# Performance work log

Measured on AMD Instinct MI355X. Metric: run time of the kernel, lower is better.

## Reference

```python
import jax, jax.numpy as jnp
import numpy as np

D_MODEL = 1024
N_HEADS = 16
D_K = D_MODEL // N_HEADS


def setup_inputs() -> dict:
    key = jax.random.key(0)
    ks = jax.random.split(key, 9)
    s = 1.0 / np.sqrt(D_MODEL)
    def lin(kw, kb):
        W = jax.random.uniform(kw, (D_MODEL, D_MODEL), jnp.float32, -s, s)
        b = jax.random.uniform(kb, (D_MODEL,), jnp.float32, -s, s)
        return W, b
    wq, bq = lin(ks[0], ks[1])
    wk, bk = lin(ks[2], ks[3])
    wv, bv = lin(ks[4], ks[5])
    wo, bo = lin(ks[6], ks[7])
    x = jax.random.normal(ks[8], (2, 2048, D_MODEL), jnp.float32)
    return {"x": x, "wq": wq, "bq": bq, "wk": wk, "bk": bk,
            "wv": wv, "bv": bv, "wo": wo, "bo": bo}


def reference(x, wq, bq, wk, bk, wv, bv, wo, bo):
    B, S, D = x.shape
    scale = 1.0 / np.sqrt(D_K)
    # projections (torch Linear: y = x W^T + b); W stored as [in,out] here
    q = x @ wq + bq
    k = x @ wk + bk
    v = x @ wv + bv
    # [B, H, S, d_k]
    q = q.reshape(B, S, N_HEADS, D_K).transpose(0, 2, 1, 3)
    k = k.reshape(B, S, N_HEADS, D_K).transpose(0, 2, 1, 3)
    v = v.reshape(B, S, N_HEADS, D_K).transpose(0, 2, 1, 3)
    scores = jnp.einsum('bhqd,bhkd->bhqk', q, k) * scale
    attn = jax.nn.softmax(scores, axis=-1)
    out = jnp.einsum('bhqk,bhkd->bhqd', attn, v)
    out = out.transpose(0, 2, 1, 3).reshape(B, S, D)
    return out @ wo + bo
```

## Files before the change

kernel.cpp:

```cpp
#include <hip/hip_runtime.h>
#include <hip/hip_bf16.h>
#include <math.h>

typedef __bf16 bf16x8 __attribute__((ext_vector_type(8)));
typedef unsigned short u16x8 __attribute__((ext_vector_type(8)));
typedef unsigned short u16x4 __attribute__((ext_vector_type(4)));
typedef float f32x4 __attribute__((ext_vector_type(4)));
typedef unsigned int u32x4 __attribute__((ext_vector_type(4)));
typedef unsigned int u32x2 __attribute__((ext_vector_type(2)));
typedef unsigned short u16;

__device__ __forceinline__ u16 f2bf(float f) {
    unsigned int x = __float_as_uint(f);
    x += 0x7fffu + ((x >> 16) & 1u);
    return (u16)(x >> 16);
}
__device__ __forceinline__ void glds16(const void* g, void* l) {
    __builtin_amdgcn_global_load_lds(
        (const __attribute__((address_space(1))) void*)g,
        (__attribute__((address_space(3))) void*)l, 16, 0, 0);
}
__device__ __forceinline__ void swap_half(unsigned& a, unsigned& b) {
    u32x2 t = __builtin_amdgcn_permlane32_swap(a, b, false, false);
    t = __builtin_amdgcn_permlane16_swap(t[0], t[1], false, false);
    a = t[0]; b = t[1];
}

__global__ __launch_bounds__(256) void prep(const float* __restrict__ W0, const float* __restrict__ W1,
                                            const float* __restrict__ W2, const float* __restrict__ W3,
                                            const float* __restrict__ X,
                                            u16* __restrict__ Wt, u16* __restrict__ Xb) {
    int z = blockIdx.z;
    if (z >= 4) {
        int row = (z - 4) * 1024 + blockIdx.y * 32 + blockIdx.x;
        const float* src = X + (size_t)row * 1024 + threadIdx.x * 4;
        f32x4 v = *(const f32x4*)src;
        u16x4 o; o[0] = f2bf(v[0]); o[1] = f2bf(v[1]); o[2] = f2bf(v[2]); o[3] = f2bf(v[3]);
        *(u16x4*)&Xb[(size_t)row * 1024 + threadIdx.x * 4] = o;
        return;
    }
    __shared__ float T[32][33];
    const float* W = (z == 0) ? W0 : ((z == 1) ? W1 : ((z == 2) ? W2 : W3));
    u16* dst = Wt + (size_t)z * 1024 * 1024;
    int k0 = blockIdx.y * 32, n0 = blockIdx.x * 32;
    int x = threadIdx.x & 31, y0 = threadIdx.x >> 5;
#pragma unroll
    for (int i = 0; i < 4; i++) {
        int y = y0 + i * 8;
        T[y][x] = W[(size_t)(k0 + y) * 1024 + n0 + x];
    }
    __syncthreads();
#pragma unroll
    for (int i = 0; i < 4; i++) {
        int y = y0 + i * 8;
        dst[(size_t)(n0 + y) * 1024 + k0 + x] = f2bf(T[x][y]);
    }
}

__global__ __launch_bounds__(512, 2) void gemm256(
    const u16* __restrict__ Bt,
    const float* __restrict__ b0, const float* __restrict__ b1, const float* __restrict__ b2,
    const u16* __restrict__ A, u16* __restrict__ C, u16* __restrict__ Vt)
{
    __shared__ __align__(16) u16 As[2][256 * 64];
    __shared__ __align__(16) u16 Bs[2][256 * 64];
    int tid = threadIdx.x;
    int lane = tid & 63, l15 = lane & 15, quad = lane >> 4;
    int wid = tid >> 6;
    int wm = wid >> 2, wn = wid & 3;
    int m0 = blockIdx.y * 256, n0 = blockIdx.x * 256;
    int sel = n0 >> 10;
    const float* bias = (sel == 0) ? b0 : ((sel == 1) ? b1 : b2);

    f32x4 acc[8][4];
#pragma unroll
    for (int i = 0; i < 8; i++)
#pragma unroll
        for (int j = 0; j < 4; j++) { f32x4 z = {0.f, 0.f, 0.f, 0.f}; acc[i][j] = z; }

    int rr = lane >> 3;
    int cc = (lane & 7) ^ rr;
    int fs7 = l15 & 7;
    const u16* abase = A  + (size_t)m0 * 1024;
    const u16* bbase = Bt + (size_t)n0 * 1024;

    auto stage = [&](int kt, int hp, int buf) {
        const u16* gsrc = (hp < 2) ? abase : bbase;
        u16* ldst = (hp < 2) ? As[buf] : Bs[buf];
        int k0 = kt * 64;
        int hbase = (hp & 1) * 128;
#pragma unroll
        for (int inst = 0; inst < 2; inst++) {
            int r0 = hbase + wid * 16 + inst * 8;
            glds16(&gsrc[(size_t)(r0 + rr) * 1024 + k0 + cc * 8], &ldst[r0 * 64]);
        }
    };

#pragma unroll
    for (int hp = 0; hp < 4; hp++) stage(0, hp, 0);

#pragma unroll 2
    for (int it = 0; it < 16; ++it) {
        int c = it & 1;
        if (it < 15) {
            stage(it + 1, 0, c ^ 1);
            asm volatile("s_waitcnt vmcnt(2)");
        } else {
            asm volatile("s_waitcnt vmcnt(0)");
        }
        __builtin_amdgcn_s_barrier();
        bf16x8 bfr[4][2];
#pragma unroll
        for (int nt = 0; nt < 4; nt++)
#pragma unroll
            for (int h = 0; h < 2; h++)
                bfr[nt][h] = *(const bf16x8*)&Bs[c][(wn * 64 + nt * 16 + l15) * 64 +
                                                    ((((h << 2) | quad) ^ fs7) * 8)];
        {
            bf16x8 af[2][2];
#pragma unroll
            for (int m = 0; m < 2; m++)
#pragma unroll
                for (int h = 0; h < 2; h++)
                    af[m][h] = *(const bf16x8*)&As[c][(wm * 128 + m * 16 + l15) * 64 +
                                                      ((((h << 2) | quad) ^ fs7) * 8)];
            asm volatile("s_waitcnt lgkmcnt(0)");
            __builtin_amdgcn_sched_barrier(0);
            __builtin_amdgcn_s_setprio(1);
#pragma unroll
            for (int m = 0; m < 2; m++)
#pragma unroll
                for (int nt = 0; nt < 4; nt++)
#pragma unroll
                    for (int h = 0; h < 2; h++)
                        acc[m][nt] = __builtin_amdgcn_mfma_f32_16x16x32_bf16(
                            af[m][h], bfr[nt][h], acc[m][nt], 0, 0, 0);
            __builtin_amdgcn_s_setprio(0);
            __builtin_amdgcn_s_barrier();
        }
#pragma unroll
        for (int p = 1; p < 4; p++) {
            bf16x8 af[2][2];
#pragma unroll
            for (int m = 0; m < 2; m++)
#pragma unroll
                for (int h = 0; h < 2; h++)
                    af[m][h] = *(const bf16x8*)&As[c][(wm * 128 + (p * 2 + m) * 16 + l15) * 64 +
                                                      ((((h << 2) | quad) ^ fs7) * 8)];
            if (it < 15) stage(it + 1, p, c ^ 1);
            __builtin_amdgcn_s_barrier();
            asm volatile("s_waitcnt lgkmcnt(0)");
            __builtin_amdgcn_sched_barrier(0);
            __builtin_amdgcn_s_setprio(1);
#pragma unroll
            for (int m = 0; m < 2; m++)
#pragma unroll
                for (int nt = 0; nt < 4; nt++)
#pragma unroll
                    for (int h = 0; h < 2; h++)
                        acc[p * 2 + m][nt] = __builtin_amdgcn_mfma_f32_16x16x32_bf16(
                            af[m][h], bfr[nt][h], acc[p * 2 + m][nt], 0, 0, 0);
            __builtin_amdgcn_s_setprio(0);
            __builtin_amdgcn_s_barrier();
        }
    }

    if (sel == 2) {
        int b = m0 >> 11;
#pragma unroll
        for (int mt = 0; mt < 8; mt++) {
            int gr = m0 + wm * 128 + mt * 16 + quad * 4;
            int s = gr & 2047;
#pragma unroll
            for (int nt = 0; nt < 4; nt++) {
                int gcl = (n0 & 1023) + wn * 64 + nt * 16 + l15;
                float bb = bias[gcl];
                u16x4 pk;
#pragma unroll
                for (int r = 0; r < 4; r++) pk[r] = f2bf(acc[mt][nt][r] + bb);
                *(u16x4*)&Vt[(size_t)((b * 16 + (gcl >> 6)) * 64 + (gcl & 63)) * 2048 + s] = pk;
            }
        }
        return;
    }
    float qs = (sel == 0) ? 0.18033688011112f : 1.0f;
#pragma unroll
    for (int mt = 0; mt < 8; mt++) {
        int gr = m0 + wm * 128 + mt * 16 + quad * 4;
#pragma unroll
        for (int nt = 0; nt < 4; nt++) {
            int gc = n0 + wn * 64 + nt * 16 + l15;
            float bb = bias[gc & 1023];
#pragma unroll
            for (int r = 0; r < 4; r++)
                C[(size_t)(gr + r) * 3072 + gc] = f2bf((acc[mt][nt][r] + bb) * qs);
        }
    }
}

template <bool OF32, bool VSPLIT>
__global__ __launch_bounds__(256) void gemm(
    const u16* __restrict__ Bt,
    const float* __restrict__ b0, const float* __restrict__ b1, const float* __restrict__ b2,
    const u16* __restrict__ A, void* __restrict__ Cptr, u16* __restrict__ Vt, int Ntot)
{
    __shared__ __align__(16) u16 As[128 * 32];
    __shared__ __align__(16) u16 Bs[128 * 32];
    int tid = threadIdx.x;
    int lane = tid & 63, l15 = lane & 15, quad = lane >> 4;
    int wid = tid >> 6, wm = wid >> 1, wn = wid & 1;
    int m0 = blockIdx.y * 128, n0 = blockIdx.x * 128;
    int sel = n0 >> 10;
    const float* bias = (sel == 0) ? b0 : ((sel == 1) ? b1 : b2);

    f32x4 acc[4][4];
#pragma unroll
    for (int i = 0; i < 4; i++)
#pragma unroll
        for (int j = 0; j < 4; j++) { f32x4 z = {0.f, 0.f, 0.f, 0.f}; acc[i][j] = z; }

    int rr = lane >> 2;
    int cc = (lane & 3) ^ ((rr >> 1) & 3);
    const u16* abase = A  + (size_t)m0 * 1024;
    const u16* bbase = Bt + (size_t)n0 * 1024;
    int fsw = (l15 >> 1) & 3;

    for (int k0 = 0; k0 < 1024; k0 += 32) {
#pragma unroll
        for (int inst = 0; inst < 2; inst++) {
            int r0 = wid * 32 + inst * 16;
            glds16(&abase[(size_t)(r0 + rr) * 1024 + k0 + cc * 8], &As[r0 * 32]);
            glds16(&bbase[(size_t)(r0 + rr) * 1024 + k0 + cc * 8], &Bs[r0 * 32]);
        }
        __syncthreads();
        bf16x8 af[4], bf[4];
#pragma unroll
        for (int mt = 0; mt < 4; mt++)
            af[mt] = *(const bf16x8*)&As[(wm * 64 + mt * 16 + l15) * 32 + ((quad ^ fsw) * 8)];
#pragma unroll
        for (int nt = 0; nt < 4; nt++)
            bf[nt] = *(const bf16x8*)&Bs[(wn * 64 + nt * 16 + l15) * 32 + ((quad ^ fsw) * 8)];
#pragma unroll
        for (int mt = 0; mt < 4; mt++)
#pragma unroll
            for (int nt = 0; nt < 4; nt++)
                acc[mt][nt] = __builtin_amdgcn_mfma_f32_16x16x32_bf16(af[mt], bf[nt], acc[mt][nt], 0, 0, 0);
        __syncthreads();
    }
    if (VSPLIT && sel == 2) {
        int b = m0 >> 11;
#pragma unroll
        for (int mt = 0; mt < 4; mt++) {
            int gr = m0 + wm * 64 + mt * 16 + quad * 4;
            int s = gr & 2047;
#pragma unroll
            for (int nt = 0; nt < 4; nt++) {
                int gcl = (n0 & 1023) + wn * 64 + nt * 16 + l15;
                float bb = bias[gcl];
                u16x4 pk;
#pragma unroll
                for (int r = 0; r < 4; r++) pk[r] = f2bf(acc[mt][nt][r] + bb);
                *(u16x4*)&Vt[(size_t)((b * 16 + (gcl >> 6)) * 64 + (gcl & 63)) * 2048 + s] = pk;
            }
        }
        return;
    }
    float qs = (VSPLIT && sel == 0) ? 0.18033688011112f : 1.0f;
#pragma unroll
    for (int mt = 0; mt < 4; mt++) {
        int gr = m0 + wm * 64 + mt * 16 + quad * 4;
#pragma unroll
        for (int nt = 0; nt < 4; nt++) {
            int gc = n0 + wn * 64 + nt * 16 + l15;
            float bb = bias[gc & 1023];
#pragma unroll
            for (int r = 0; r < 4; r++) {
                float v = (acc[mt][nt][r] + bb) * qs;
                if (OF32) ((float*)Cptr)[(size_t)(gr + r) * Ntot + gc] = v;
                else      ((u16*)Cptr)[(size_t)(gr + r) * Ntot + gc] = f2bf(v);
            }
        }
    }
}

__global__ __launch_bounds__(256, 2) void attn(const u16* __restrict__ QKV,
                                               const u16* __restrict__ Vt,
                                               u16* __restrict__ O)
{
    __shared__ __align__(16) u16 Ks[4][64 * 64];
    __shared__ __align__(16) u16 Vs[4][64 * 64];
    const int S = 2048, DQ = 3072;
    int tid = threadIdx.x, wid = tid >> 6, lane = tid & 63;
    int l15 = lane & 15, quad = lane >> 4;
    int lin = blockIdx.x;
    int xcd = lin & 7;
    int rest = lin >> 3;
    int qt = rest & 15;
    int g = xcd + 8 * (rest >> 4);
    int h = g & 15, b = g >> 4;
    const u16* base = QKV + (size_t)b * S * DQ + h * 64;
    const u16* Kb = base + 1024;
    const u16* Vtb = Vt + (size_t)((b * 16 + h) * 64) * 2048;
    int q0 = qt * 128 + wid * 32;

    bf16x8 qA0 = *(const bf16x8*)&base[(size_t)(q0 + l15) * DQ + quad * 8];
    bf16x8 qA1 = *(const bf16x8*)&base[(size_t)(q0 + l15) * DQ + 32 + quad * 8];
    bf16x8 qB0 = *(const bf16x8*)&base[(size_t)(q0 + 16 + l15) * DQ + quad * 8];
    bf16x8 qB1 = *(const bf16x8*)&base[(size_t)(q0 + 16 + l15) * DQ + 32 + quad * 8];

    f32x4 oA[4], oB[4];
#pragma unroll
    for (int i = 0; i < 4; i++) { f32x4 z = {0.f, 0.f, 0.f, 0.f}; oA[i] = z; oB[i] = z; }
    float psA = 0.f, psB = 0.f;

    int rr = lane >> 3;
    int cc = (lane & 7) ^ rr;
    int fs7 = l15 & 7;

    auto stage = [&](int it, int bsel) {
        int kv0 = it << 6;
#pragma unroll
        for (int inst = 0; inst < 2; inst++) {
            int r0 = wid * 16 + inst * 8;
            glds16(&Kb[(size_t)(kv0 + r0 + rr) * DQ + cc * 8], &Ks[bsel][r0 * 64]);
            glds16(&Vtb[(size_t)(r0 + rr) * 2048 + kv0 + cc * 8], &Vs[bsel][r0 * 64]);
        }
    };

    stage(0, 0);
    stage(1, 1);
    for (int it = 0; it < 32; ++it) {
        int cb = it & 3;
        if (it < 30) {
            stage(it + 2, (it + 2) & 3);
            asm volatile("s_waitcnt vmcnt(8)");
        } else if (it == 30) {
            asm volatile("s_waitcnt vmcnt(4)");
        } else {
            asm volatile("s_waitcnt vmcnt(0)");
        }
        __builtin_amdgcn_s_barrier();

        const u16* Kc = &Ks[cb][0];
        const u16* Vc = &Vs[cb][0];
        bf16x8 kfa[4], kfb[4], vfa[4], vfb[4];
#pragma unroll
        for (int t = 0; t < 4; t++) {
            kfa[t] = *(const bf16x8*)&Kc[(t * 16 + l15) * 64 + ((quad ^ fs7) * 8)];
            kfb[t] = *(const bf16x8*)&Kc[(t * 16 + l15) * 64 + (((quad + 4) ^ fs7) * 8)];
        }
#pragma unroll
        for (int dt = 0; dt < 4; dt++) {
            vfa[dt] = *(const bf16x8*)&Vc[(dt * 16 + l15) * 64 + ((quad ^ fs7) * 8)];
            vfb[dt] = *(const bf16x8*)&Vc[(dt * 16 + l15) * 64 + (((quad + 4) ^ fs7) * 8)];
        }

        f32x4 sA[4], sB[4];
#pragma unroll
        for (int t = 0; t < 4; t++) { f32x4 z = {0.f, 0.f, 0.f, 0.f}; sA[t] = z; sB[t] = z; }
        __builtin_amdgcn_s_setprio(1);
#pragma unroll
        for (int t = 0; t < 4; t++) {
            sA[t] = __builtin_amdgcn_mfma_f32_16x16x32_bf16(kfa[t], qA0, sA[t], 0, 0, 0);
            sA[t] = __builtin_amdgcn_mfma_f32_16x16x32_bf16(kfb[t], qA1, sA[t], 0, 0, 0);
            sB[t] = __builtin_amdgcn_mfma_f32_16x16x32_bf16(kfa[t], qB0, sB[t], 0, 0, 0);
            sB[t] = __builtin_amdgcn_mfma_f32_16x16x32_bf16(kfb[t], qB1, sB[t], 0, 0, 0);
        }
        __builtin_amdgcn_s_setprio(0);

        unsigned wA[4][2], wB[4][2];
#pragma unroll
        for (int t = 0; t < 4; t++) {
            float a0 = __builtin_amdgcn_exp2f(sA[t][0]);
            float a1 = __builtin_amdgcn_exp2f(sA[t][1]);
            float a2 = __builtin_amdgcn_exp2f(sA[t][2]);
            float a3 = __builtin_amdgcn_exp2f(sA[t][3]);
            psA += (a0 + a1) + (a2 + a3);
            asm("v_cvt_pk_bf16_f32 %0, %1, %2" : "=v"(wA[t][0]) : "v"(a0), "v"(a1));
            asm("v_cvt_pk_bf16_f32 %0, %1, %2" : "=v"(wA[t][1]) : "v"(a2), "v"(a3));
            float b0_ = __builtin_amdgcn_exp2f(sB[t][0]);
            float b1_ = __builtin_amdgcn_exp2f(sB[t][1]);
            float b2_ = __builtin_amdgcn_exp2f(sB[t][2]);
            float b3_ = __builtin_amdgcn_exp2f(sB[t][3]);
            psB += (b0_ + b1_) + (b2_ + b3_);
            asm("v_cvt_pk_bf16_f32 %0, %1, %2" : "=v"(wB[t][0]) : "v"(b0_), "v"(b1_));
            asm("v_cvt_pk_bf16_f32 %0, %1, %2" : "=v"(wB[t][1]) : "v"(b2_), "v"(b3_));
        }
        unsigned a0 = wA[0][0], a2 = wA[1][0]; swap_half(a0, a2);
        unsigned a1 = wA[0][1], a3 = wA[1][1]; swap_half(a1, a3);
        unsigned c0 = wA[2][0], c2 = wA[3][0]; swap_half(c0, c2);
        unsigned c1 = wA[2][1], c3 = wA[3][1]; swap_half(c1, c3);
        u32x4 pdA0 = {a0, a1, a2, a3};
        u32x4 pdA1 = {c0, c1, c2, c3};
        bf16x8 pfA0 = *(bf16x8*)&pdA0;
        bf16x8 pfA1 = *(bf16x8*)&pdA1;
        unsigned d0 = wB[0][0], d2 = wB[1][0]; swap_half(d0, d2);
        unsigned d1 = wB[0][1], d3 = wB[1][1]; swap_half(d1, d3);
        unsigned e0 = wB[2][0], e2 = wB[3][0]; swap_half(e0, e2);
        unsigned e1 = wB[2][1], e3 = wB[3][1]; swap_half(e1, e3);
        u32x4 pdB0 = {d0, d1, d2, d3};
        u32x4 pdB1 = {e0, e1, e2, e3};
        bf16x8 pfB0 = *(bf16x8*)&pdB0;
        bf16x8 pfB1 = *(bf16x8*)&pdB1;

        __builtin_amdgcn_s_setprio(1);
#pragma unroll
        for (int dt = 0; dt < 4; dt++) {
            oA[dt] = __builtin_amdgcn_mfma_f32_16x16x32_bf16(pfA0, vfa[dt], oA[dt], 0, 0, 0);
            oA[dt] = __builtin_amdgcn_mfma_f32_16x16x32_bf16(pfA1, vfb[dt], oA[dt], 0, 0, 0);
            oB[dt] = __builtin_amdgcn_mfma_f32_16x16x32_bf16(pfB0, vfa[dt], oB[dt], 0, 0, 0);
            oB[dt] = __builtin_amdgcn_mfma_f32_16x16x32_bf16(pfB1, vfb[dt], oB[dt], 0, 0, 0);
        }
        __builtin_amdgcn_s_setprio(0);
    }

    psA += __shfl_xor(psA, 16);
    psA += __shfl_xor(psA, 32);
    psB += __shfl_xor(psB, 16);
    psB += __shfl_xor(psB, 32);
#pragma unroll
    for (int r = 0; r < 4; r++) {
        float invA = 1.0f / __shfl(psA, quad * 4 + r);
        size_t rowA = (size_t)(b * S + q0 + quad * 4 + r);
#pragma unroll
        for (int dt = 0; dt < 4; dt++)
            O[rowA * 1024 + h * 64 + dt * 16 + l15] = f2bf(oA[dt][r] * invA);
        float invB = 1.0f / __shfl(psB, quad * 4 + r);
        size_t rowB = rowA + 16;
#pragma unroll
        for (int dt = 0; dt < 4; dt++)
            O[rowB * 1024 + h * 64 + dt * 16 + l15] = f2bf(oB[dt][r] * invB);
    }
}

extern "C" void kernel_launch(void* const* d_in, const int* in_sizes, int n_in,
                              void* d_out, int out_size, void* d_ws, size_t ws_size,
                              hipStream_t stream) {
    const float* x  = (const float*)d_in[0];
    const float* wq = (const float*)d_in[1];
    const float* bq = (const float*)d_in[2];
    const float* wk = (const float*)d_in[3];
    const float* bk = (const float*)d_in[4];
    const float* wv = (const float*)d_in[5];
    const float* bv = (const float*)d_in[6];
    const float* wo = (const float*)d_in[7];
    const float* bo = (const float*)d_in[8];
    float* out = (float*)d_out;

    u16* qkv  = (u16*)d_ws;
    u16* obuf = qkv  + (size_t)4096 * 3072;
    u16* vt   = obuf + (size_t)4096 * 1024;
    u16* wt   = vt   + (size_t)2048 * 2048;
    u16* xb   = wt   + (size_t)4 * 1024 * 1024;

    dim3 tb(256);
    prep<<<dim3(32, 32, 8), tb, 0, stream>>>(wq, wk, wv, wo, x, wt, xb);
    gemm256<<<dim3(12, 16), dim3(512), 0, stream>>>(wt, bq, bk, bv, xb, qkv, vt);
    attn<<<dim3(512), tb, 0, stream>>>(qkv, vt, obuf);
    gemm<true, false><<<dim3(8, 32), tb, 0, stream>>>(wt + (size_t)3 * 1024 * 1024,
                                                      bo, bo, bo, obuf, out, (u16*)nullptr, 1024);
}
```

Before: 193.2 us.

## Software-pipeline QK^T of next KV tile with softmax and PV of current tile

Splits the attention loop body into a QK^T stage and an exp/pack/PV stage, then interleaves them so the score MFMAs for tile i+1 are issued alongside the softmax and PV MFMAs for tile i. Two score accumulator sets alternate between even and odd tiles, and the loop is unrolled by two with a prologue and an epilogue. The aim is to hide the exp and permute latency and the MFMA dependency stalls behind independent matrix work. The cost is roughly double the score registers, which may lower occupancy, and more intricate waitcnt and barrier bookkeeping across the four LDS buffers.

```diff
diff --git a/kernel.cpp b/kernel.cpp
--- a/kernel.cpp
+++ b/kernel.cpp
@@ -317,8 +317,8 @@
     int cc = (lane & 7) ^ rr;
     int fs7 = l15 & 7;
 
-    auto stage = [&](int it, int bsel) {
-        int kv0 = it << 6;
+    auto stage = [&](int t) {
+        int kv0 = t << 6, bsel = t & 3;
 #pragma unroll
         for (int inst = 0; inst < 2; inst++) {
             int r0 = wid * 16 + inst * 8;
@@ -327,61 +327,49 @@
         }
     };
 
-    stage(0, 0);
-    stage(1, 1);
-    for (int it = 0; it < 32; ++it) {
-        int cb = it & 3;
-        if (it < 30) {
-            stage(it + 2, (it + 2) & 3);
-            asm volatile("s_waitcnt vmcnt(8)");
-        } else if (it == 30) {
-            asm volatile("s_waitcnt vmcnt(4)");
-        } else {
-            asm volatile("s_waitcnt vmcnt(0)");
-        }
-        __builtin_amdgcn_s_barrier();
-
-        const u16* Kc = &Ks[cb][0];
-        const u16* Vc = &Vs[cb][0];
-        bf16x8 kfa[4], kfb[4], vfa[4], vfb[4];
+    auto qk = [&](int i, f32x4* s) {
+        const u16* Kc = &Ks[i & 3][0];
+        bf16x8 kfa[4], kfb[4];
 #pragma unroll
         for (int t = 0; t < 4; t++) {
             kfa[t] = *(const bf16x8*)&Kc[(t * 16 + l15) * 64 + ((quad ^ fs7) * 8)];
             kfb[t] = *(const bf16x8*)&Kc[(t * 16 + l15) * 64 + (((quad + 4) ^ fs7) * 8)];
         }
 #pragma unroll
+        for (int t = 0; t < 8; t++) { f32x4 z = {0.f, 0.f, 0.f, 0.f}; s[t] = z; }
+        __builtin_amdgcn_s_setprio(1);
+#pragma unroll
+        for (int t = 0; t < 4; t++) {
+            s[t]     = __builtin_amdgcn_mfma_f32_16x16x32_bf16(kfa[t], qA0, s[t], 0, 0, 0);
+            s[t]     = __builtin_amdgcn_mfma_f32_16x16x32_bf16(kfb[t], qA1, s[t], 0, 0, 0);
+            s[4 + t] = __builtin_amdgcn_mfma_f32_16x16x32_bf16(kfa[t], qB0, s[4 + t], 0, 0, 0);
+            s[4 + t] = __builtin_amdgcn_mfma_f32_16x16x32_bf16(kfb[t], qB1, s[4 + t], 0, 0, 0);
+        }
+        __builtin_amdgcn_s_setprio(0);
+    };
+
+    auto fin = [&](int i, f32x4* s) {
+        const u16* Vc = &Vs[i & 3][0];
+        bf16x8 vfa[4], vfb[4];
+#pragma unroll
         for (int dt = 0; dt < 4; dt++) {
             vfa[dt] = *(const bf16x8*)&Vc[(dt * 16 + l15) * 64 + ((quad ^ fs7) * 8)];
             vfb[dt] = *(const bf16x8*)&Vc[(dt * 16 + l15) * 64 + (((quad + 4) ^ fs7) * 8)];
         }
-
-        f32x4 sA[4], sB[4];
-#pragma unroll
-        for (int t = 0; t < 4; t++) { f32x4 z = {0.f, 0.f, 0.f, 0.f}; sA[t] = z; sB[t] = z; }
-        __builtin_amdgcn_s_setprio(1);
+        unsigned wA[4][2], wB[4][2];
 #pragma unroll
         for (int t = 0; t < 4; t++) {
-            sA[t] = __builtin_amdgcn_mfma_f32_16x16x32_bf16(kfa[t], qA0, sA[t], 0, 0, 0);
-            sA[t] = __builtin_amdgcn_mfma_f32_16x16x32_bf16(kfb[t], qA1, sA[t], 0, 0, 0);
-            sB[t] = __builtin_amdgcn_mfma_f32_16x16x32_bf16(kfa[t], qB0, sB[t], 0, 0, 0);
-            sB[t] = __builtin_amdgcn_mfma_f32_16x16x32_bf16(kfb[t], qB1, sB[t], 0, 0, 0);
-        }
-        __builtin_amdgcn_s_setprio(0);
-
-        unsigned wA[4][2], wB[4][2];
-#pragma unroll
-        for (int t = 0; t < 4; t++) {
-            float a0 = __builtin_amdgcn_exp2f(sA[t][0]);
-            float a1 = __builtin_amdgcn_exp2f(sA[t][1]);
-            float a2 = __builtin_amdgcn_exp2f(sA[t][2]);
-            float a3 = __builtin_amdgcn_exp2f(sA[t][3]);
+            float a0 = __builtin_amdgcn_exp2f(s[t][0]);
+            float a1 = __builtin_amdgcn_exp2f(s[t][1]);
+            float a2 = __builtin_amdgcn_exp2f(s[t][2]);
+            float a3 = __builtin_amdgcn_exp2f(s[t][3]);
             psA += (a0 + a1) + (a2 + a3);
             asm("v_cvt_pk_bf16_f32 %0, %1, %2" : "=v"(wA[t][0]) : "v"(a0), "v"(a1));
             asm("v_cvt_pk_bf16_f32 %0, %1, %2" : "=v"(wA[t][1]) : "v"(a2), "v"(a3));
-            float b0_ = __builtin_amdgcn_exp2f(sB[t][0]);
-            float b1_ = __builtin_amdgcn_exp2f(sB[t][1]);
-            float b2_ = __builtin_amdgcn_exp2f(sB[t][2]);
-            float b3_ = __builtin_amdgcn_exp2f(sB[t][3]);
+            float b0_ = __builtin_amdgcn_exp2f(s[4 + t][0]);
+            float b1_ = __builtin_amdgcn_exp2f(s[4 + t][1]);
+            float b2_ = __builtin_amdgcn_exp2f(s[4 + t][2]);
+            float b3_ = __builtin_amdgcn_exp2f(s[4 + t][3]);
             psB += (b0_ + b1_) + (b2_ + b3_);
             asm("v_cvt_pk_bf16_f32 %0, %1, %2" : "=v"(wB[t][0]) : "v"(b0_), "v"(b1_));
             asm("v_cvt_pk_bf16_f32 %0, %1, %2" : "=v"(wB[t][1]) : "v"(b2_), "v"(b3_));
@@ -402,7 +390,6 @@
         u32x4 pdB1 = {e0, e1, e2, e3};
         bf16x8 pfB0 = *(bf16x8*)&pdB0;
         bf16x8 pfB1 = *(bf16x8*)&pdB1;
-
         __builtin_amdgcn_s_setprio(1);
 #pragma unroll
         for (int dt = 0; dt < 4; dt++) {
@@ -412,7 +399,33 @@
             oB[dt] = __builtin_amdgcn_mfma_f32_16x16x32_bf16(pfB1, vfb[dt], oB[dt], 0, 0, 0);
         }
         __builtin_amdgcn_s_setprio(0);
-    }
+    };
+
+    f32x4 sE[8], sO[8];
+
+    stage(0); stage(1);
+    asm volatile("s_waitcnt vmcnt(4)");
+    __builtin_amdgcn_s_barrier();
+    stage(2);
+    qk(0, sE);
+    for (int j = 0; j < 15; ++j) {
+        int i = 2 * j + 1;
+        asm volatile("s_waitcnt vmcnt(4)");
+        __builtin_amdgcn_s_barrier();
+        if (i + 2 < 32) stage(i + 2);
+        qk(i, sO);
+        fin(i - 1, sE);
+        asm volatile("s_waitcnt vmcnt(4)");
+        __builtin_amdgcn_s_barrier();
+        if (i + 3 < 32) stage(i + 3);
+        qk(i + 1, sE);
+        fin(i, sO);
+    }
+    asm volatile("s_waitcnt vmcnt(0)");
+    __builtin_amdgcn_s_barrier();
+    qk(31, sO);
+    fin(30, sE);
+    fin(31, sO);
 
     psA += __shfl_xor(psA, 16);
     psA += __shfl_xor(psA, 32);
```

Result: no change. 194.3 us (+0.6%).
